# Performance work log

Measured on AMD Instinct MI355X. Metric: run time of the kernel, lower is better.

The kernel has to match this reference:

```python
import jax, jax.numpy as jnp
import numpy as np

B, S, D = 32, 8192, 64


def setup_inputs() -> dict:
    key = jax.random.key(0)
    k1, k2 = jax.random.split(key)
    input_real = jax.random.normal(k1, (B, S, D), dtype=jnp.float32)
    input_imag = jax.random.normal(k2, (B, S, D), dtype=jnp.float32)
    return {"input_real": input_real, "input_imag": input_imag}


def reference(input_real, input_imag):
    # ComplexMixture: mean over seq of per-token complex outer products v v^H.
    # Original builds [B,S,D,D] via 4 batch_dots then means over S; fused here
    # as Gram contractions over the sequence axis (no [B,S,D,D] intermediate).
    seq_len = input_real.shape[1]
    inv_s = jnp.asarray(1.0 / seq_len, dtype=input_real.dtype)
    rr = jnp.einsum('bsi,bsj->bij', input_real, input_real)
    ii = jnp.einsum('bsi,bsj->bij', input_imag, input_imag)
    ri = jnp.einsum('bsi,bsj->bij', input_real, input_imag)
    out_real = (rr + ii) * inv_s                     # [B, D, D], symmetric
    out_imag = (ri - jnp.swapaxes(ri, 1, 2)) * inv_s  # [B, D, D], antisymmetric
    return (out_real, out_imag)
```

## Files before the change

### kernel.cpp

```cpp
#include <hip/hip_runtime.h>


#define BATCH 32
#define SEQ   8192
#define DD    64
#define BK    128

typedef __bf16 bf16x8 __attribute__((ext_vector_type(8)));
typedef float  f32x16 __attribute__((ext_vector_type(16)));

__device__ __forceinline__ unsigned bf16pk(float a, float b) {
  unsigned ua = __builtin_bit_cast(unsigned, a);
  unsigned ub = __builtin_bit_cast(unsigned, b);
  ua = (ua + 0x7fffu + ((ua >> 16) & 1u)) >> 16;
  ub = (ub + 0x7fffu + ((ub >> 16) & 1u)) >> 16;
  return (ua & 0xffffu) | (ub << 16);
}

template<int CHUNKS>
__global__ __launch_bounds__(256, 4) void gram_partial(
    const float* __restrict__ R, const float* __restrict__ I,
    float* __restrict__ ws)
{
  constexpr int SCHUNK = SEQ / CHUNKS;
  constexpr int NIT    = SCHUNK / BK;
  __shared__ uint4 lds[32][64];
  const int tid  = threadIdx.x;
  const int wave = tid >> 6;
  const int lane = tid & 63;
  const int b = blockIdx.x & 31;
  const int c = blockIdx.x >> 5;
  const float* Rb = R + (size_t)b * (SEQ * DD);
  const float* Ib = I + (size_t)b * (SEQ * DD);
  const int m0 = (wave >> 1) * 32;
  const int n0 = (wave & 1) * 32;
  const int l31 = lane & 31;
  const int lhi = lane >> 5;

  f32x16 accR = {};
  f32x16 accI = {};

  const int chunk0 = c * SCHUNK;

  for (int it = 0; it < NIT; ++it) {
    const int sbase = chunk0 + it * BK;
    float rv[4][8], iv[4][8];
    #pragma unroll
    for (int gi = 0; gi < 4; ++gi) {
      const int g = gi * 4 + wave;
      const float* pR = Rb + (size_t)(sbase + g * 8) * DD + lane;
      const float* pI = Ib + (size_t)(sbase + g * 8) * DD + lane;
      #pragma unroll
      for (int j = 0; j < 8; ++j) { rv[gi][j] = pR[j * 64]; iv[gi][j] = pI[j * 64]; }
    }
    #pragma unroll
    for (int gi = 0; gi < 4; ++gi) {
      const int g = gi * 4 + wave;
      uint4 qR; qR.x = bf16pk(rv[gi][0], rv[gi][1]); qR.y = bf16pk(rv[gi][2], rv[gi][3]);
                qR.z = bf16pk(rv[gi][4], rv[gi][5]); qR.w = bf16pk(rv[gi][6], rv[gi][7]);
      uint4 qI; qI.x = bf16pk(iv[gi][0], iv[gi][1]); qI.y = bf16pk(iv[gi][2], iv[gi][3]);
                qI.z = bf16pk(iv[gi][4], iv[gi][5]); qI.w = bf16pk(iv[gi][6], iv[gi][7]);
      lds[g][lane]      = qR;
      lds[16 + g][lane] = qI;
    }
    __syncthreads();
    #pragma unroll
    for (int ks = 0; ks < BK / 16; ++ks) {
      const int kg = ks * 2 + lhi;
      bf16x8 aR = __builtin_bit_cast(bf16x8, lds[kg][m0 + l31]);
      bf16x8 bR = __builtin_bit_cast(bf16x8, lds[kg][n0 + l31]);
      bf16x8 aI = __builtin_bit_cast(bf16x8, lds[16 + kg][m0 + l31]);
      bf16x8 bI = __builtin_bit_cast(bf16x8, lds[16 + kg][n0 + l31]);
      accR = __builtin_amdgcn_mfma_f32_32x32x16_bf16(aR, bR, accR, 0, 0, 0);
      accR = __builtin_amdgcn_mfma_f32_32x32x16_bf16(aI, bI, accR, 0, 0, 0);
      accI = __builtin_amdgcn_mfma_f32_32x32x16_bf16(aR, bI, accI, 0, 0, 0);
    }
    __syncthreads();
  }

  float* wsR = ws + ((size_t)(c * 32 + b) * 2) * 4096;
  float* wsM = wsR + 4096;
  const int jj = n0 + l31;
  #pragma unroll
  for (int r = 0; r < 16; ++r) {
    const int i = m0 + (r & 3) + 8 * (r >> 2) + 4 * lhi;
    wsR[i * 64 + jj] = accR[r];
  }
  float* ldsf = (float*)lds;
  #pragma unroll
  for (int r = 0; r < 16; ++r) {
    const int i = m0 + (r & 3) + 8 * (r >> 2) + 4 * lhi;
    ldsf[i * 65 + jj] = accI[r];
  }
  __syncthreads();
  #pragma unroll
  for (int k = 0; k < 16; ++k) {
    const int e = tid + 256 * k;
    const int i = e >> 6, j = e & 63;
    wsM[e] = ldsf[i * 65 + j] - ldsf[j * 65 + i];
  }
}

template<int CHUNKS>
__global__ __launch_bounds__(256) void gram_reduce(
    const float4* __restrict__ ws, float4* __restrict__ out)
{
  const int o = blockIdx.x * 256 + threadIdx.x;
  const int kind = o >> 15;
  const int rem  = o & 32767;
  const int b    = rem >> 10;
  const int e    = rem & 1023;
  const float inv = 1.0f / (float)SEQ;
  float sx = 0.f, sy = 0.f, sz = 0.f, sw = 0.f;
  #pragma unroll
  for (int c = 0; c < CHUNKS; ++c) {
    float4 v = ws[((size_t)(c * 32 + b) * 2 + kind) * 1024 + e];
    sx += v.x; sy += v.y; sz += v.z; sw += v.w;
  }
  float4 r; r.x = sx * inv; r.y = sy * inv; r.z = sz * inv; r.w = sw * inv;
  out[o] = r;
}

extern "C" void kernel_launch(void* const* d_in, const int* in_sizes, int n_in,
                              void* d_out, int out_size, void* d_ws, size_t ws_size,
                              hipStream_t stream) {
  const float* R = (const float*)d_in[0];
  const float* I = (const float*)d_in[1];
  float* out = (float*)d_out;
  float* ws  = (float*)d_ws;

  const size_t need32 = (size_t)32 * 32 * 2 * 4096 * 4;
  if (ws_size >= need32) {
    gram_partial<32><<<BATCH * 32, 256, 0, stream>>>(R, I, ws);
    gram_reduce<32><<<256, 256, 0, stream>>>((const float4*)ws, (float4*)out);
  } else {
    gram_partial<16><<<BATCH * 16, 256, 0, stream>>>(R, I, ws);
    gram_reduce<16><<<256, 256, 0, stream>>>((const float4*)ws, (float4*)out);
  }
}
```

Measured before the change: 161.6 us.

## Load fp32 tiles directly into LDS and exploit Gram symmetry across waves

Replaces per-thread scalar global loads and register-side bf16 packing with 16-byte global_load_lds transfers that write fp32 tiles straight into shared memory. Each wave converts its fragments to bf16 on the LDS read path. Work is re-split across the four waves so the symmetric real Gram only computes three of its four 32x32 blocks, and the missing block is read transposed at write-out. The K tile shrinks to 64 rows to fit fp32 tiles in LDS. In exchange, LDS reads become eight strided scalar loads per fragment, conversion work is repeated per wave, and the MFMA load across waves is uneven.

```diff
diff --git a/kernel.cpp b/kernel.cpp
--- a/kernel.cpp
+++ b/kernel.cpp
@@ -4,10 +4,15 @@
 #define BATCH 32
 #define SEQ   8192
 #define DD    64
-#define BK    128
+#define BK    64
 
 typedef __bf16 bf16x8 __attribute__((ext_vector_type(8)));
 typedef float  f32x16 __attribute__((ext_vector_type(16)));
+
+#define GLD_LDS16(gp, lp) \
+  __builtin_amdgcn_global_load_lds( \
+      (const __attribute__((address_space(1))) void*)(gp), \
+      (__attribute__((address_space(3))) void*)(lp), 16, 0, 0)
 
 __device__ __forceinline__ unsigned bf16pk(float a, float b) {
   unsigned ua = __builtin_bit_cast(unsigned, a);
@@ -17,6 +22,17 @@
   return (ua & 0xffffu) | (ub << 16);
 }
 
+__device__ __forceinline__ bf16x8 ldsfrag(const float* p) {
+  float f0 = p[0*64], f1 = p[1*64], f2 = p[2*64], f3 = p[3*64];
+  float f4 = p[4*64], f5 = p[5*64], f6 = p[6*64], f7 = p[7*64];
+  uint4 q;
+  q.x = bf16pk(f0, f1); q.y = bf16pk(f2, f3);
+  q.z = bf16pk(f4, f5); q.w = bf16pk(f6, f7);
+  return __builtin_bit_cast(bf16x8, q);
+}
+
+#define MFMA(a, b, c) __builtin_amdgcn_mfma_f32_32x32x16_bf16((a), (b), (c), 0, 0, 0)
+
 template<int CHUNKS>
 __global__ __launch_bounds__(256, 4) void gram_partial(
     const float* __restrict__ R, const float* __restrict__ I,
@@ -24,80 +40,94 @@
 {
   constexpr int SCHUNK = SEQ / CHUNKS;
   constexpr int NIT    = SCHUNK / BK;
-  __shared__ uint4 lds[32][64];
+  __shared__ float lds[8320];
+  float* ldsR = lds;
+  float* ldsI = lds + 4096;
+
   const int tid  = threadIdx.x;
   const int wave = tid >> 6;
   const int lane = tid & 63;
+  const int l31  = lane & 31;
+  const int lhi  = lane >> 5;
   const int b = blockIdx.x & 31;
   const int c = blockIdx.x >> 5;
   const float* Rb = R + (size_t)b * (SEQ * DD);
   const float* Ib = I + (size_t)b * (SEQ * DD);
-  const int m0 = (wave >> 1) * 32;
-  const int n0 = (wave & 1) * 32;
-  const int l31 = lane & 31;
-  const int lhi = lane >> 5;
 
-  f32x16 accR = {};
-  f32x16 accI = {};
+  f32x16 acc0 = {};
+  f32x16 acc1 = {};
 
   const int chunk0 = c * SCHUNK;
 
   for (int it = 0; it < NIT; ++it) {
-    const int sbase = chunk0 + it * BK;
-    float rv[4][8], iv[4][8];
+    const float* gR = Rb + (size_t)(chunk0 + it * BK) * DD;
+    const float* gI = Ib + (size_t)(chunk0 + it * BK) * DD;
     #pragma unroll
-    for (int gi = 0; gi < 4; ++gi) {
-      const int g = gi * 4 + wave;
-      const float* pR = Rb + (size_t)(sbase + g * 8) * DD + lane;
-      const float* pI = Ib + (size_t)(sbase + g * 8) * DD + lane;
-      #pragma unroll
-      for (int j = 0; j < 8; ++j) { rv[gi][j] = pR[j * 64]; iv[gi][j] = pI[j * 64]; }
-    }
-    #pragma unroll
-    for (int gi = 0; gi < 4; ++gi) {
-      const int g = gi * 4 + wave;
-      uint4 qR; qR.x = bf16pk(rv[gi][0], rv[gi][1]); qR.y = bf16pk(rv[gi][2], rv[gi][3]);
-                qR.z = bf16pk(rv[gi][4], rv[gi][5]); qR.w = bf16pk(rv[gi][6], rv[gi][7]);
-      uint4 qI; qI.x = bf16pk(iv[gi][0], iv[gi][1]); qI.y = bf16pk(iv[gi][2], iv[gi][3]);
-                qI.z = bf16pk(iv[gi][4], iv[gi][5]); qI.w = bf16pk(iv[gi][6], iv[gi][7]);
-      lds[g][lane]      = qR;
-      lds[16 + g][lane] = qI;
+    for (int t = 0; t < 4; ++t) {
+      const int row0 = wave * 16 + t * 4;
+      GLD_LDS16(gR + row0 * 64 + lane * 4, &ldsR[row0 * 64]);
+      GLD_LDS16(gI + row0 * 64 + lane * 4, &ldsI[row0 * 64]);
     }
     __syncthreads();
     #pragma unroll
-    for (int ks = 0; ks < BK / 16; ++ks) {
-      const int kg = ks * 2 + lhi;
-      bf16x8 aR = __builtin_bit_cast(bf16x8, lds[kg][m0 + l31]);
-      bf16x8 bR = __builtin_bit_cast(bf16x8, lds[kg][n0 + l31]);
-      bf16x8 aI = __builtin_bit_cast(bf16x8, lds[16 + kg][m0 + l31]);
-      bf16x8 bI = __builtin_bit_cast(bf16x8, lds[16 + kg][n0 + l31]);
-      accR = __builtin_amdgcn_mfma_f32_32x32x16_bf16(aR, bR, accR, 0, 0, 0);
-      accR = __builtin_amdgcn_mfma_f32_32x32x16_bf16(aI, bI, accR, 0, 0, 0);
-      accI = __builtin_amdgcn_mfma_f32_32x32x16_bf16(aR, bI, accI, 0, 0, 0);
+    for (int ks = 0; ks < 4; ++ks) {
+      const int kb = (ks * 16 + lhi * 8) * 64 + l31;
+      const float* pR = &ldsR[kb];
+      const float* pI = &ldsI[kb];
+      if (wave == 0) {
+        bf16x8 r0 = ldsfrag(pR), i0 = ldsfrag(pI);
+        acc0 = MFMA(r0, r0, acc0);
+        acc0 = MFMA(i0, i0, acc0);
+        acc1 = MFMA(r0, i0, acc1);
+      } else if (wave == 1) {
+        bf16x8 r0 = ldsfrag(pR), r32 = ldsfrag(pR + 32);
+        bf16x8 i0 = ldsfrag(pI), i32 = ldsfrag(pI + 32);
+        acc0 = MFMA(r0, r32, acc0);
+        acc0 = MFMA(i0, i32, acc0);
+      } else if (wave == 2) {
+        bf16x8 r0 = ldsfrag(pR), r32 = ldsfrag(pR + 32);
+        bf16x8 i0 = ldsfrag(pI), i32 = ldsfrag(pI + 32);
+        acc0 = MFMA(r32, i0, acc0);
+        acc1 = MFMA(r0, i32, acc1);
+      } else {
+        bf16x8 r32 = ldsfrag(pR + 32), i32 = ldsfrag(pI + 32);
+        acc0 = MFMA(r32, r32, acc0);
+        acc0 = MFMA(i32, i32, acc0);
+        acc1 = MFMA(r32, i32, acc1);
+      }
     }
     __syncthreads();
   }
 
-  float* wsR = ws + ((size_t)(c * 32 + b) * 2) * 4096;
-  float* wsM = wsR + 4096;
-  const int jj = n0 + l31;
+  float* ldsS = lds;
+  float* ldsM = lds + 4160;
+  const int jj = l31;
   #pragma unroll
   for (int r = 0; r < 16; ++r) {
-    const int i = m0 + (r & 3) + 8 * (r >> 2) + 4 * lhi;
-    wsR[i * 64 + jj] = accR[r];
-  }
-  float* ldsf = (float*)lds;
-  #pragma unroll
-  for (int r = 0; r < 16; ++r) {
-    const int i = m0 + (r & 3) + 8 * (r >> 2) + 4 * lhi;
-    ldsf[i * 65 + jj] = accI[r];
+    const int ii = (r & 3) + 8 * (r >> 2) + 4 * lhi;
+    if (wave == 0) {
+      ldsS[ii * 65 + jj]               = acc0[r];
+      ldsM[ii * 65 + jj]               = acc1[r];
+    } else if (wave == 1) {
+      ldsS[ii * 65 + 32 + jj]          = acc0[r];
+    } else if (wave == 2) {
+      ldsM[(32 + ii) * 65 + jj]        = acc0[r];
+      ldsM[ii * 65 + 32 + jj]          = acc1[r];
+    } else {
+      ldsS[(32 + ii) * 65 + 32 + jj]   = acc0[r];
+      ldsM[(32 + ii) * 65 + 32 + jj]   = acc1[r];
+    }
   }
   __syncthreads();
+  float* wsS = ws + ((size_t)(c * 32 + b) * 2) * 4096;
+  float* wsM = wsS + 4096;
   #pragma unroll
   for (int k = 0; k < 16; ++k) {
     const int e = tid + 256 * k;
     const int i = e >> 6, j = e & 63;
-    wsM[e] = ldsf[i * 65 + j] - ldsf[j * 65 + i];
+    const float sv = (i >= 32 && j < 32) ? ldsS[j * 65 + i] : ldsS[i * 65 + j];
+    wsS[e] = sv;
+    wsM[e] = ldsM[i * 65 + j] - ldsM[j * 65 + i];
   }
 }
 
```

New measurement: 171.9 us. +6.4%, slower.
